# Kernel optimization log

Hardware: AMD Instinct MI355X
Metric: run time of the kernel (lower is better)

Reference implementation:

```python
import jax, jax.numpy as jnp
import numpy as np

jax.config.update("jax_enable_x64", True)

_FULL = 1 << 32
_MASK = _FULL - 1
_HALF = _FULL >> 1
_QUARTER = _HALF >> 1
_THREE_QUARTER = 3 * _QUARTER


def setup_inputs() -> dict:
    key = jax.random.key(0)
    num_symbols = 262144            # e.g. a 512x512 plane of {-1,+1} symbols
    num_bits = 2 * num_symbols      # compressed payload, ~2 bits/symbol budget
    payload_bits = jax.random.randint(key, (num_bits,), 0, 2, dtype=jnp.int64)
    return {
        "payload_bits": payload_bits,
        "total_freq": 4096,         # 1 << frequency_precision (12)
        "num_symbols": num_symbols,
        "context_bits": 8,
    }


def reference(payload_bits, total_freq, num_symbols, context_bits):
    bits = payload_bits.astype(jnp.int64)
    nb = bits.shape[0]
    num_states = 1 << context_bits
    smask = num_states - 1

    def read_bit(ptr):
        # _BitReader returns 0 past the end of the payload
        return jnp.where(ptr < nb, bits[jnp.clip(ptr, 0, nb - 1)], jnp.int64(0))

    # initial 32-bit code word
    idx32 = jnp.arange(32, dtype=jnp.int64)
    b32 = jnp.where(idx32 < nb, bits[jnp.clip(idx32, 0, nb - 1)], 0)
    code0 = jnp.sum(b32 << (31 - idx32))

    def renorm(carry):
        # E1/E2/E3 renormalization loop (bit-level, data dependent)
        def cond(c):
            low, high, code, ptr = c
            return (high < _HALF) | (low >= _HALF) | ((low >= _QUARTER) & (high < _THREE_QUARTER))

        def body(c):
            low, high, code, ptr = c
            sub = jnp.where(high < _HALF, jnp.int64(0),
                            jnp.where(low >= _HALF, jnp.int64(_HALF), jnp.int64(_QUARTER)))
            low = low - sub
            high = high - sub
            code = code - sub
            low = (low << 1) & _MASK
            high = ((high << 1) & _MASK) | 1
            code = ((code << 1) & _MASK) | read_bit(ptr)
            return (low, high, code, ptr + 1)

        return jax.lax.while_loop(cond, body, carry)

    def step(carry, _):
        low, high, code, ptr, state, count0, count1 = carry
        n0 = count0[state]
        n1 = count1[state]
        total = n0 + n1
        p0 = n0.astype(jnp.float64) / total.astype(jnp.float64)
        p0_freq = jnp.clip(jnp.rint(p0 * (total_freq - 2)) + 1.0, 1.0, float(total_freq - 1)).astype(jnp.int64)
        rng = high - low + 1                      # fits int64 (<= 2^32)
        scaled = ((code - low + 1) * total_freq - 1) // rng
        split = low + rng * p0_freq // total_freq
        bit = (scaled >= p0_freq).astype(jnp.int64)
        low2 = jnp.where(bit == 0, low, split)
        high2 = jnp.where(bit == 0, split - 1, high)
        low3, high3, code3, ptr3 = renorm((low2, high2, code, ptr))
        count0 = count0.at[state].add(1 - bit)
        count1 = count1.at[state].add(bit)
        state2 = ((state << 1) | bit) & smask
        return (low3, high3, code3, ptr3, state2, count0, count1), bit

    init = (
        jnp.int64(0),               # low
        jnp.int64(_MASK),           # high = 2^32 - 1
        code0.astype(jnp.int64),    # code
        jnp.int64(32),              # bit pointer (32 bits consumed)
        jnp.int64(0),               # context state
        jnp.ones(num_states, dtype=jnp.int64),  # count0 (Laplace init)
        jnp.ones(num_states, dtype=jnp.int64),  # count1
    )
    _, out_bits = jax.lax.scan(step, init, None, length=num_symbols)
    # map {0,1} -> {-1,+1} float32 symbols (reshape to bitstream.shape is metadata-only)
    return out_bits.astype(jnp.float32) * 2.0 - 1.0
```

## Files before the change

kernel.cpp:

```cpp
#include <hip/hip_runtime.h>


#define WORDS_LDS 16400
#define MAX_STATES 1024
#define OBITS_WORDS 8192

__device__ __forceinline__ long long ddiv_floor(long long n, long long d) {
    double qd = (double)n / (double)d;
    long long q = (long long)qd;
    long long r = n - q * d;
    q -= (r < 0);
    q += (r >= d);
    return q;
}

template<bool FAST>
__device__ __forceinline__ void decode_serial(
    const unsigned* __restrict__ words, unsigned* tab, unsigned* obits,
    const int* __restrict__ bits, int nb, int nwords,
    unsigned total_freq, int tf_shift, int num_symbols, int smask,
    unsigned pf0, float* __restrict__ out)
{
    const unsigned H = 0x80000000u;
    unsigned low = 0u, high = 0xFFFFFFFFu;
    unsigned code = words[0];
    unsigned long long bitbuf = (((unsigned long long)words[1]) << 32) | (unsigned long long)words[2];
    int navail = 64;
    unsigned pre = words[3];
    int widx = 4;

    const double tfm2d = (double)(total_freq - 2u);
    const int tfm1 = (int)(total_freq - 1u);
    const unsigned tfm2_2 = (total_freq - 2u) << 1;
    constexpr int EXT = FAST ? 14 : 30;

    int state = 0;
    unsigned n0 = 1u, n1 = 1u, pf = pf0;

    int wIdx = 0;
    unsigned wN0 = 1u, wN1 = 1u, wPf = pf0;

    unsigned obuf = 0u;

    for (int s = 0; s < num_symbols; ++s) {
        const int c0 = (state << 1) & smask;
        uint4 q = *reinterpret_cast<const uint4*>(tab + 2 * c0);

        if (navail <= 32) {
            bitbuf |= ((unsigned long long)pre) << (32 - navail);
            navail += 32;
            unsigned nxt = 0u;
            if (widx < WORDS_LDS) {
                nxt = words[widx];
            } else if (widx < nwords) {
                unsigned g = 0u;
                long long base = ((long long)widx) << 5;
                for (int j = 0; j < 32; ++j) {
                    long long idx = base + j;
                    int b = (idx < (long long)nb) ? (bits[idx] & 1) : 0;
                    g |= ((unsigned)b) << (31 - j);
                }
                nxt = g;
            }
            pre = nxt;
            ++widx;
        }

        const unsigned rngm1 = high - low;
        const unsigned long long P = (unsigned long long)pf * rngm1 + pf;
        const unsigned soff = FAST ? (unsigned)(P >> tf_shift)
                                   : (unsigned)ddiv_floor((long long)P, (long long)total_freq);
        const unsigned dlt = code - low;
        const int bit = (dlt >= soff) ? 1 : 0;
        const unsigned split = low + soff;
        low  = bit ? split : low;
        high = bit ? high : (split - 1u);
        obuf = (obuf << 1) | (unsigned)bit;

        const unsigned nn0 = n0 + (unsigned)(1 - bit);
        const unsigned nn1 = n1 + (unsigned)bit;
        unsigned pfn;
        if (FAST) {
            const unsigned t  = nn0 + nn1;
            const unsigned d2 = t << 1;
            const unsigned num2 = __umul24(tfm2_2, nn0) + t;
            const float qf = (float)num2 * __builtin_amdgcn_rcpf((float)d2);
            unsigned qi = (unsigned)qf;
            int r = (int)(num2 - __umul24(qi, d2));
            if (r < 0)          { qi -= 1u; r += (int)d2; }
            if (r >= (int)d2)   { qi += 1u; r -= (int)d2; }
            pfn = qi + 1u;
            if (__builtin_expect(r == 0, 0)) {
                asm volatile("");
                double p0d = (double)(int)nn0 / (double)(int)t;
                double pfd = rint(p0d * tfm2d) + 1.0;
                int pfi = (int)pfd;
                pfi = pfi < 1 ? 1 : (pfi > tfm1 ? tfm1 : pfi);
                pfn = (unsigned)pfi;
            }
        } else {
            double p0d = (double)(int)nn0 / (double)(int)(nn0 + nn1);
            double pfd = rint(p0d * tfm2d) + 1.0;
            int pfi = (int)pfd;
            pfi = pfi < 1 ? 1 : (pfi > tfm1 ? tfm1 : pfi);
            pfn = (unsigned)pfi;
        }

        const unsigned x = low ^ high;
        const int k = __builtin_clz(x);
        const unsigned aa = ~(low << (k + 1));
        const unsigned bb = (high << (k + 1)) | ((2u << k) - 1u);
        const int m = __builtin_clz(aa | bb);
        const int K = k + m;
        const unsigned sub = (m != 0) ? H : 0u;
        const unsigned ones = (1u << K) - 1u;
        const unsigned tE = (unsigned)(bitbuf >> (64 - EXT));
        const unsigned tK = tE >> (EXT - K);
        low  = (low << K) - sub;
        high = (high << K) + ones - sub;
        code = ((code << K) | tK) - sub;
        bitbuf <<= K;
        navail -= K;

        const int nidx = c0 | bit;
        const unsigned sw0 = bit ? q.z : q.x;
        const unsigned sw1 = bit ? q.w : q.y;
        const bool f2 = (nidx == wIdx);
        unsigned xn0 = f2 ? wN0 : sw0;
        unsigned xn1 = f2 ? wN1 : (sw1 & 0xFFFFFu);
        unsigned xpf = f2 ? wPf : (sw1 >> 20);

        *reinterpret_cast<uint2*>(tab + 2 * wIdx) = make_uint2(wN0, wN1 | (wPf << 20));
        wIdx = state; wN0 = nn0; wN1 = nn1; wPf = pfn;

        if (__builtin_expect(nidx == state, 0)) {
            asm volatile("");
            xn0 = nn0; xn1 = nn1; xpf = pfn;
        }
        state = nidx;
        n0 = xn0; n1 = xn1; pf = xpf;

        if ((s & 31) == 31) {
            int wo = s >> 5;
            if (wo < OBITS_WORDS) {
                obits[wo] = obuf;
            } else {
                int base = s & ~31;
                for (int j = 0; j < 32; ++j)
                    out[base + j] = ((obuf >> (31 - j)) & 1u) ? 1.0f : -1.0f;
            }
        }
    }
    if (num_symbols & 31) {
        int rem = num_symbols & 31;
        unsigned v = obuf << (32 - rem);
        int wo = num_symbols >> 5;
        if (wo < OBITS_WORDS) {
            obits[wo] = v;
        } else {
            int base = num_symbols & ~31;
            for (int j = 0; j < rem; ++j)
                out[base + j] = ((v >> (31 - j)) & 1u) ? 1.0f : -1.0f;
        }
    }
}

__global__ __launch_bounds__(256)
void EntropyDecoder_84928683311460_kernel(
    const int* __restrict__ bits,
    const int* __restrict__ tf_p,
    const int* __restrict__ ns_p,
    const int* __restrict__ cb_p,
    float* __restrict__ out,
    int nb)
{
    __shared__ unsigned words[WORDS_LDS];
    __shared__ __align__(16) unsigned tab[MAX_STATES * 2];
    __shared__ unsigned obits[OBITS_WORDS];

    const int tid = threadIdx.x;
    const unsigned total_freq = (unsigned)(*tf_p);
    const int num_symbols = *ns_p;
    const int context_bits = *cb_p;
    const int num_states = 1 << context_bits;
    const int smask = num_states - 1;
    const int nwords = (nb + 31) >> 5;

    for (int w = tid; w < WORDS_LDS; w += blockDim.x) {
        unsigned v = 0;
        int base = w << 5;
        if (base + 32 <= nb) {
            #pragma unroll
            for (int j = 0; j < 32; j += 4) {
                int4 b4 = *reinterpret_cast<const int4*>(bits + base + j);
                v |= ((unsigned)(b4.x & 1) << (31 - j))
                   | ((unsigned)(b4.y & 1) << (30 - j))
                   | ((unsigned)(b4.z & 1) << (29 - j))
                   | ((unsigned)(b4.w & 1) << (28 - j));
            }
        } else if (base < nb) {
            for (int j = 0; j < 32; ++j) {
                int idx = base + j;
                int b = (idx < nb) ? (bits[idx] & 1) : 0;
                v |= ((unsigned)b) << (31 - j);
            }
        }
        words[w] = v;
    }
    unsigned pf0;
    {
        double pfd = rint(0.5 * (double)(total_freq - 2u)) + 1.0;
        int t = (int)pfd;
        int tfm1 = (int)(total_freq - 1u);
        t = t < 1 ? 1 : (t > tfm1 ? tfm1 : t);
        pf0 = (unsigned)t;
    }
    for (int st = tid; st < num_states; st += blockDim.x) {
        tab[2 * st]     = 1u;
        tab[2 * st + 1] = 1u | (pf0 << 20);
    }
    __syncthreads();

    if (tid == 0) {
        const int tf_shift = 31 - __builtin_clz(total_freq);
        const bool pow2 = (total_freq & (total_freq - 1u)) == 0u;
        const unsigned long long bound =
            2ull * (unsigned long long)(total_freq - 2u) * (unsigned long long)(num_symbols + 1)
            + (unsigned long long)(num_symbols + 2);
        const bool fast = pow2 && total_freq >= 8u && total_freq <= 4096u
                          && bound < (1ull << 31);
        if (fast)
            decode_serial<true >(words, tab, obits, bits, nb, nwords, total_freq,
                                 tf_shift, num_symbols, smask, pf0, out);
        else
            decode_serial<false>(words, tab, obits, bits, nb, nwords, total_freq,
                                 tf_shift, num_symbols, smask, pf0, out);
    }
    __syncthreads();

    const int nwout = (num_symbols + 31) >> 5;
    const int npk = nwout < OBITS_WORDS ? nwout : OBITS_WORDS;
    for (int w = tid; w < npk; w += blockDim.x) {
        unsigned v = obits[w];
        int base = w << 5;
        if (base + 32 <= num_symbols) {
            #pragma unroll
            for (int j = 0; j < 32; j += 4) {
                float4 o;
                o.x = ((v >> (31 - j)) & 1u) ? 1.0f : -1.0f;
                o.y = ((v >> (30 - j)) & 1u) ? 1.0f : -1.0f;
                o.z = ((v >> (29 - j)) & 1u) ? 1.0f : -1.0f;
                o.w = ((v >> (28 - j)) & 1u) ? 1.0f : -1.0f;
                *reinterpret_cast<float4*>(out + base + j) = o;
            }
        } else {
            for (int j = 0; j < 32 && base + j < num_symbols; ++j)
                out[base + j] = ((v >> (31 - j)) & 1u) ? 1.0f : -1.0f;
        }
    }
}

extern "C" void kernel_launch(void* const* d_in, const int* in_sizes, int n_in,
                              void* d_out, int out_size, void* d_ws, size_t ws_size,
                              hipStream_t stream) {
    const int* bits = (const int*)d_in[0];
    const int* tf   = (const int*)d_in[1];
    const int* ns   = (const int*)d_in[2];
    const int* cb   = (const int*)d_in[3];
    float* out = (float*)d_out;
    int nb = in_sizes[0];

    hipLaunchKernelGGL(EntropyDecoder_84928683311460_kernel,
                       dim3(1), dim3(256), 0, stream,
                       bits, tf, ns, cb, out, nb);
}
```

Baseline: 79.84 ms.

## Keep context count table in wavefront registers via readlane instead of LDS

The fast path now runs on a full 64-lane wavefront. The 256-entry context count table is spread across lane registers (4 per lane) and read with readlane instead of LDS loads, with the pending write applied by a lane-select predicate on the next iteration. The decoder also tracks code-minus-low directly, which drops one subtraction from the serial chain. This targets LDS load latency on the serial per-symbol dependency chain. In exchange it adds 8 readlanes and selects per symbol, and it only applies when there are at most 256 states.

```diff
diff --git a/kernel.cpp b/kernel.cpp
--- a/kernel.cpp
+++ b/kernel.cpp
@@ -14,11 +14,160 @@
     return q;
 }
 
-template<bool FAST>
-__device__ __forceinline__ void decode_serial(
+__device__ __forceinline__ void decode_fast(
+    const unsigned* __restrict__ words, unsigned* obits,
+    const int* __restrict__ bits, int nb, int nwords,
+    unsigned total_freq, int tf_shift, int num_symbols, int smask,
+    unsigned pf0, float* __restrict__ out)
+{
+    const unsigned myLane = threadIdx.x & 63u;
+
+    unsigned a0 = 1u, a1 = 1u, a2 = 1u, a3 = 1u;
+    const unsigned bini = 1u | (pf0 << 20);
+    unsigned b0 = bini, b1 = bini, b2 = bini, b3 = bini;
+
+    unsigned low = 0u, high = 0xFFFFFFFFu;
+    unsigned dlt = words[0];
+    unsigned long long bitbuf = (((unsigned long long)words[1]) << 32)
+                              | (unsigned long long)words[2];
+    int unavail = 64;
+    unsigned pre = words[3];
+    int uwidx = 4;
+
+    const unsigned tfm2_2 = (total_freq - 2u) << 1;
+    const double tfm2d = (double)(total_freq - 2u);
+    const int tfm1 = (int)(total_freq - 1u);
+
+    int ustate = 0;
+    unsigned obuf = 0u;
+
+    bool pm0 = false, pm1 = false, pm2 = false, pm3 = false;
+    unsigned pN0 = 0u, pPK = 0u;
+
+    for (int s = 0; s < num_symbols; ++s) {
+        a0 = pm0 ? pN0 : a0;  a1 = pm1 ? pN0 : a1;
+        a2 = pm2 ? pN0 : a2;  a3 = pm3 ? pN0 : a3;
+        b0 = pm0 ? pPK : b0;  b1 = pm1 ? pPK : b1;
+        b2 = pm2 ? pPK : b2;  b3 = pm3 ? pPK : b3;
+
+        const int lane = ustate & 63;
+        const int ridx = ustate >> 6;
+        const unsigned ra0 = (unsigned)__builtin_amdgcn_readlane((int)a0, lane);
+        const unsigned ra1 = (unsigned)__builtin_amdgcn_readlane((int)a1, lane);
+        const unsigned ra2 = (unsigned)__builtin_amdgcn_readlane((int)a2, lane);
+        const unsigned ra3 = (unsigned)__builtin_amdgcn_readlane((int)a3, lane);
+        const unsigned rb0 = (unsigned)__builtin_amdgcn_readlane((int)b0, lane);
+        const unsigned rb1 = (unsigned)__builtin_amdgcn_readlane((int)b1, lane);
+        const unsigned rb2 = (unsigned)__builtin_amdgcn_readlane((int)b2, lane);
+        const unsigned rb3 = (unsigned)__builtin_amdgcn_readlane((int)b3, lane);
+        const unsigned rn0 = (ridx & 2) ? ((ridx & 1) ? ra3 : ra2)
+                                        : ((ridx & 1) ? ra1 : ra0);
+        const unsigned rpk = (ridx & 2) ? ((ridx & 1) ? rb3 : rb2)
+                                        : ((ridx & 1) ? rb1 : rb0);
+        const unsigned upf = rpk >> 20;
+        const unsigned un1 = rpk & 0xFFFFFu;
+
+        const unsigned rngm1 = high - low;
+        const unsigned long long P = (unsigned long long)upf * rngm1 + upf;
+        const unsigned soff = (unsigned)(P >> tf_shift);
+        const bool bt = (dlt >= soff);
+        const unsigned bitv = bt ? 1u : 0u;
+        const unsigned split = low + soff;
+        low  = bt ? split : low;
+        high = bt ? high : (split - 1u);
+        dlt  = bt ? (dlt - soff) : dlt;
+        obuf = (obuf << 1) | bitv;
+
+        const unsigned nn0 = rn0 + 1u - bitv;
+        const unsigned nn1 = un1 + bitv;
+        const unsigned t  = nn0 + nn1;
+        const unsigned d2 = t << 1;
+        const unsigned num2 = __umul24(tfm2_2, nn0) + t;
+        const float qf = (float)num2 * __builtin_amdgcn_rcpf((float)d2);
+        unsigned qi = (unsigned)qf;
+        int r = (int)(num2 - __umul24(qi, d2));
+        if (r < 0)        { qi -= 1u; r += (int)d2; }
+        if (r >= (int)d2) { qi += 1u; r -= (int)d2; }
+        unsigned pfn = qi + 1u;
+        if (__builtin_expect(__builtin_amdgcn_readfirstlane(r) == 0, 0)) {
+            double p0d = (double)(int)nn0 / (double)(int)t;
+            double pfd = rint(p0d * tfm2d) + 1.0;
+            int pfi = (int)pfd;
+            pfi = pfi < 1 ? 1 : (pfi > tfm1 ? tfm1 : pfi);
+            pfn = (unsigned)pfi;
+        }
+
+        const unsigned x = low ^ high;
+        const int k = __builtin_clz(x);
+        const unsigned aa  = ~(low << (k + 1));
+        const unsigned bbv = (high << (k + 1)) | ((2u << k) - 1u);
+        const int m = __builtin_clz(aa | bbv);
+        const int K = k + m;
+        const unsigned sub = (m != 0) ? 0x80000000u : 0u;
+        const unsigned ones = (1u << K) - 1u;
+        const unsigned tE = (unsigned)(bitbuf >> 50);
+        const unsigned tK = tE >> (14 - K);
+        low  = (low << K) - sub;
+        high = (high << K) + ones - sub;
+        dlt  = (dlt << K) | tK;
+        bitbuf <<= K;
+
+        const bool sel = (myLane == (unsigned)lane);
+        pm0 = sel && (ridx == 0);  pm1 = sel && (ridx == 1);
+        pm2 = sel && (ridx == 2);  pm3 = sel && (ridx == 3);
+        pN0 = nn0;
+        pPK = nn1 | (pfn << 20);
+
+        const int ubit = __builtin_amdgcn_readfirstlane((int)bitv);
+        ustate = ((ustate << 1) | ubit) & smask;
+        unavail -= __builtin_amdgcn_readfirstlane(K);
+        if (unavail <= 32) {
+            bitbuf |= ((unsigned long long)pre) << (32 - unavail);
+            unavail += 32;
+            unsigned nxt = 0u;
+            if (uwidx < WORDS_LDS) {
+                nxt = words[uwidx];
+            } else if (uwidx < nwords) {
+                unsigned g = 0u;
+                long long base = ((long long)uwidx) << 5;
+                for (int j = 0; j < 32; ++j) {
+                    long long idx = base + j;
+                    int b = (idx < (long long)nb) ? (bits[idx] & 1) : 0;
+                    g |= ((unsigned)b) << (31 - j);
+                }
+                nxt = g;
+            }
+            pre = nxt;
+            ++uwidx;
+        }
+        if ((s & 31) == 31) {
+            int wo = s >> 5;
+            if (wo < OBITS_WORDS) {
+                obits[wo] = obuf;
+            } else {
+                int base = s & ~31;
+                for (int j = 0; j < 32; ++j)
+                    out[base + j] = ((obuf >> (31 - j)) & 1u) ? 1.0f : -1.0f;
+            }
+        }
+    }
+    if (num_symbols & 31) {
+        int rem = num_symbols & 31;
+        unsigned v = obuf << (32 - rem);
+        int wo = num_symbols >> 5;
+        if (wo < OBITS_WORDS) obits[wo] = v;
+        else {
+            int base = num_symbols & ~31;
+            for (int j = 0; j < rem; ++j)
+                out[base + j] = ((v >> (31 - j)) & 1u) ? 1.0f : -1.0f;
+        }
+    }
+}
+
+__device__ void decode_serial_slow(
     const unsigned* __restrict__ words, unsigned* tab, unsigned* obits,
     const int* __restrict__ bits, int nb, int nwords,
-    unsigned total_freq, int tf_shift, int num_symbols, int smask,
+    unsigned total_freq, int num_symbols, int smask,
     unsigned pf0, float* __restrict__ out)
 {
     const unsigned H = 0x80000000u;
@@ -31,28 +180,22 @@
 
     const double tfm2d = (double)(total_freq - 2u);
     const int tfm1 = (int)(total_freq - 1u);
-    const unsigned tfm2_2 = (total_freq - 2u) << 1;
-    constexpr int EXT = FAST ? 14 : 30;
 
     int state = 0;
     unsigned n0 = 1u, n1 = 1u, pf = pf0;
-
     int wIdx = 0;
     unsigned wN0 = 1u, wN1 = 1u, wPf = pf0;
-
     unsigned obuf = 0u;
 
     for (int s = 0; s < num_symbols; ++s) {
         const int c0 = (state << 1) & smask;
         uint4 q = *reinterpret_cast<const uint4*>(tab + 2 * c0);
-
         if (navail <= 32) {
             bitbuf |= ((unsigned long long)pre) << (32 - navail);
             navail += 32;
             unsigned nxt = 0u;
-            if (widx < WORDS_LDS) {
-                nxt = words[widx];
-            } else if (widx < nwords) {
+            if (widx < WORDS_LDS) nxt = words[widx];
+            else if (widx < nwords) {
                 unsigned g = 0u;
                 long long base = ((long long)widx) << 5;
                 for (int j = 0; j < 32; ++j) {
@@ -65,11 +208,9 @@
             pre = nxt;
             ++widx;
         }
-
         const unsigned rngm1 = high - low;
         const unsigned long long P = (unsigned long long)pf * rngm1 + pf;
-        const unsigned soff = FAST ? (unsigned)(P >> tf_shift)
-                                   : (unsigned)ddiv_floor((long long)P, (long long)total_freq);
+        const unsigned soff = (unsigned)ddiv_floor((long long)P, (long long)total_freq);
         const unsigned dlt = code - low;
         const int bit = (dlt >= soff) ? 1 : 0;
         const unsigned split = low + soff;
@@ -79,43 +220,22 @@
 
         const unsigned nn0 = n0 + (unsigned)(1 - bit);
         const unsigned nn1 = n1 + (unsigned)bit;
-        unsigned pfn;
-        if (FAST) {
-            const unsigned t  = nn0 + nn1;
-            const unsigned d2 = t << 1;
-            const unsigned num2 = __umul24(tfm2_2, nn0) + t;
-            const float qf = (float)num2 * __builtin_amdgcn_rcpf((float)d2);
-            unsigned qi = (unsigned)qf;
-            int r = (int)(num2 - __umul24(qi, d2));
-            if (r < 0)          { qi -= 1u; r += (int)d2; }
-            if (r >= (int)d2)   { qi += 1u; r -= (int)d2; }
-            pfn = qi + 1u;
-            if (__builtin_expect(r == 0, 0)) {
-                asm volatile("");
-                double p0d = (double)(int)nn0 / (double)(int)t;
-                double pfd = rint(p0d * tfm2d) + 1.0;
-                int pfi = (int)pfd;
-                pfi = pfi < 1 ? 1 : (pfi > tfm1 ? tfm1 : pfi);
-                pfn = (unsigned)pfi;
-            }
-        } else {
-            double p0d = (double)(int)nn0 / (double)(int)(nn0 + nn1);
-            double pfd = rint(p0d * tfm2d) + 1.0;
-            int pfi = (int)pfd;
-            pfi = pfi < 1 ? 1 : (pfi > tfm1 ? tfm1 : pfi);
-            pfn = (unsigned)pfi;
-        }
+        double p0d = (double)(int)nn0 / (double)(int)(nn0 + nn1);
+        double pfd = rint(p0d * tfm2d) + 1.0;
+        int pfi = (int)pfd;
+        pfi = pfi < 1 ? 1 : (pfi > tfm1 ? tfm1 : pfi);
+        unsigned pfn = (unsigned)pfi;
 
         const unsigned x = low ^ high;
         const int k = __builtin_clz(x);
         const unsigned aa = ~(low << (k + 1));
-        const unsigned bb = (high << (k + 1)) | ((2u << k) - 1u);
-        const int m = __builtin_clz(aa | bb);
+        const unsigned bbv = (high << (k + 1)) | ((2u << k) - 1u);
+        const int m = __builtin_clz(aa | bbv);
         const int K = k + m;
         const unsigned sub = (m != 0) ? H : 0u;
         const unsigned ones = (1u << K) - 1u;
-        const unsigned tE = (unsigned)(bitbuf >> (64 - EXT));
-        const unsigned tK = tE >> (EXT - K);
+        const unsigned tE = (unsigned)(bitbuf >> 34);
+        const unsigned tK = tE >> (30 - K);
         low  = (low << K) - sub;
         high = (high << K) + ones - sub;
         code = ((code << K) | tK) - sub;
@@ -129,10 +249,8 @@
         unsigned xn0 = f2 ? wN0 : sw0;
         unsigned xn1 = f2 ? wN1 : (sw1 & 0xFFFFFu);
         unsigned xpf = f2 ? wPf : (sw1 >> 20);
-
         *reinterpret_cast<uint2*>(tab + 2 * wIdx) = make_uint2(wN0, wN1 | (wPf << 20));
         wIdx = state; wN0 = nn0; wN1 = nn1; wPf = pfn;
-
         if (__builtin_expect(nidx == state, 0)) {
             asm volatile("");
             xn0 = nn0; xn1 = nn1; xpf = pfn;
@@ -142,9 +260,8 @@
 
         if ((s & 31) == 31) {
             int wo = s >> 5;
-            if (wo < OBITS_WORDS) {
-                obits[wo] = obuf;
-            } else {
+            if (wo < OBITS_WORDS) obits[wo] = obuf;
+            else {
                 int base = s & ~31;
                 for (int j = 0; j < 32; ++j)
                     out[base + j] = ((obuf >> (31 - j)) & 1u) ? 1.0f : -1.0f;
@@ -155,9 +272,8 @@
         int rem = num_symbols & 31;
         unsigned v = obuf << (32 - rem);
         int wo = num_symbols >> 5;
-        if (wo < OBITS_WORDS) {
-            obits[wo] = v;
-        } else {
+        if (wo < OBITS_WORDS) obits[wo] = v;
+        else {
             int base = num_symbols & ~31;
             for (int j = 0; j < rem; ++j)
                 out[base + j] = ((v >> (31 - j)) & 1u) ? 1.0f : -1.0f;
@@ -221,20 +337,24 @@
     }
     __syncthreads();
 
-    if (tid == 0) {
-        const int tf_shift = 31 - __builtin_clz(total_freq);
-        const bool pow2 = (total_freq & (total_freq - 1u)) == 0u;
-        const unsigned long long bound =
-            2ull * (unsigned long long)(total_freq - 2u) * (unsigned long long)(num_symbols + 1)
-            + (unsigned long long)(num_symbols + 2);
-        const bool fast = pow2 && total_freq >= 8u && total_freq <= 4096u
-                          && bound < (1ull << 31);
-        if (fast)
-            decode_serial<true >(words, tab, obits, bits, nb, nwords, total_freq,
-                                 tf_shift, num_symbols, smask, pf0, out);
-        else
-            decode_serial<false>(words, tab, obits, bits, nb, nwords, total_freq,
-                                 tf_shift, num_symbols, smask, pf0, out);
+    const int tf_shift = 31 - __builtin_clz(total_freq);
+    const bool pow2 = (total_freq & (total_freq - 1u)) == 0u;
+    const unsigned long long bound =
+        2ull * (unsigned long long)(total_freq - 2u) * (unsigned long long)(num_symbols + 1)
+        + (unsigned long long)(num_symbols + 2);
+    const bool fast = pow2 && total_freq >= 8u && total_freq <= 4096u
+                      && bound < (1ull << 31) && num_states <= 256;
+
+    if (fast) {
+        if (tid < 64) {
+            decode_fast(words, obits, bits, nb, nwords, total_freq, tf_shift,
+                        num_symbols, smask, pf0, out);
+        }
+    } else {
+        if (tid == 0) {
+            decode_serial_slow(words, tab, obits, bits, nb, nwords, total_freq,
+                               num_symbols, smask, pf0, out);
+        }
     }
     __syncthreads();
 
```

After: 87.04 ms. 1.09x slower.

## Add specialized fast serial decoder with two-step context prefetch and branchless refill

Applied to the files above, without the earlier changes.

Adds a dedicated fast decode path that prefetches both possible next-next context table entries one step ahead, so the table load leaves the serial dependency chain. The path also keeps code-minus-low directly instead of code, refills the bit buffer without branches, preloads the next word, and unrolls 32 symbols per output word. Forwarding from the previous two updates handles table read-after-write hazards. The path only runs under tighter guards on state count, symbol count and payload size, and falls back to the slow path otherwise. This adds register pressure and some correctness risk in the hazard handling.

```diff
diff --git a/kernel.cpp b/kernel.cpp
--- a/kernel.cpp
+++ b/kernel.cpp
@@ -14,11 +14,124 @@
     return q;
 }
 
-template<bool FAST>
-__device__ __forceinline__ void decode_serial(
+__device__ __forceinline__ void decode_fast(
+    const unsigned* __restrict__ words, unsigned* tab, unsigned* obits,
+    unsigned total_freq, int tf_shift, int num_symbols, int smask, unsigned pf0)
+{
+    const unsigned H = 0x80000000u;
+    unsigned low = 0u, high = 0xFFFFFFFFu;
+    unsigned dlt = words[0];
+    unsigned long long bitbuf = (((unsigned long long)words[1]) << 32)
+                              | (unsigned long long)words[2];
+    int unavail = 64;
+    unsigned pre = words[3];
+    int widx = 4;
+    unsigned wnext = words[4];
+
+    const unsigned tfm2_2 = (total_freq - 2u) << 1;
+    const double tfm2d = (double)(total_freq - 2u);
+    const int tfm1 = (int)(total_freq - 1u);
+
+    int st = 0, stP = -1;
+    unsigned entN0 = 1u, entPK = 1u | (pf0 << 20);
+    unsigned P0n0 = 1u, P0pk = entPK;
+    unsigned P1n0 = 1u, P1pk = entPK;
+    unsigned uN0p = 0u, uPKp = 0u;
+
+    const int iters = num_symbols >> 5;
+    for (int it = 0; it < iters; ++it) {
+        unsigned obuf = 0u;
+        #pragma unroll
+        for (int u = 0; u < 32; ++u) {
+            const int gbase = ((st << 2) & smask) * 2;
+            const uint4 Ga = *reinterpret_cast<const uint4*>(tab + gbase);
+            const uint4 Gb = *reinterpret_cast<const uint4*>(tab + gbase + 4);
+
+            const unsigned pf  = entPK >> 20;
+            const unsigned n1v = entPK & 0xFFFFFu;
+            const unsigned n0v = entN0;
+            const unsigned rngm1 = high - low;
+            const unsigned long long P = (unsigned long long)pf * rngm1 + pf;
+            const unsigned soff = (unsigned)(P >> tf_shift);
+            const bool bt = (dlt >= soff);
+            const unsigned bitv = bt ? 1u : 0u;
+            const unsigned split = low + soff;
+            low  = bt ? split : low;
+            high = bt ? high : (split - 1u);
+            dlt  = bt ? (dlt - soff) : dlt;
+            obuf = (obuf << 1) | bitv;
+
+            const unsigned nn0 = n0v + 1u - bitv;
+            const unsigned nn1 = n1v + bitv;
+            const unsigned tt  = nn0 + nn1;
+            const unsigned d2  = tt << 1;
+            const unsigned num2 = __umul24(tfm2_2, nn0) + tt;
+            const float qf = (float)num2 * __builtin_amdgcn_rcpf((float)d2);
+            unsigned qi = (unsigned)qf;
+            int r = (int)(num2 - __umul24(qi, d2));
+            if (r < 0)        { qi -= 1u; r += (int)d2; }
+            if (r >= (int)d2) { qi += 1u; r -= (int)d2; }
+            unsigned pfn = qi + 1u;
+            if (__builtin_expect(__builtin_amdgcn_readfirstlane(r) == 0, 0)) {
+                asm volatile("");
+                double p0d = (double)(int)nn0 / (double)(int)tt;
+                double pfd = rint(p0d * tfm2d) + 1.0;
+                int pfi = (int)pfd;
+                pfi = pfi < 1 ? 1 : (pfi > tfm1 ? tfm1 : pfi);
+                pfn = (unsigned)pfi;
+            }
+            const unsigned npk = nn1 | (pfn << 20);
+
+            const unsigned x = low ^ high;
+            const int k = __builtin_clz(x);
+            const unsigned aa   = ~(low << (k + 1));
+            const unsigned bbv2 = (high << (k + 1)) | ((2u << k) - 1u);
+            const int m = __builtin_clz(aa | bbv2);
+            const int K = k + m;
+            const unsigned sub  = (m != 0) ? H : 0u;
+            const unsigned ones = (1u << K) - 1u;
+            const unsigned tK = ((unsigned)(bitbuf >> 50)) >> (14 - K);
+            low  = (low << K) - sub;
+            high = (high << K) + ones - sub;
+            dlt  = (dlt << K) | tK;
+            bitbuf <<= K;
+            unavail -= K;
+
+            const bool need = (unavail <= 32);
+            const unsigned long long ins =
+                (((unsigned long long)pre) << 32) >> (unavail & 63);
+            bitbuf |= need ? ins : 0ull;
+            unavail += need ? 32 : 0;
+            pre = need ? wnext : pre;
+            widx += need ? 1 : 0;
+            const int widxc = widx < (WORDS_LDS - 1) ? widx : (WORDS_LDS - 1);
+            wnext = words[widxc];
+
+            *reinterpret_cast<uint2*>(tab + 2 * st) = make_uint2(nn0, npk);
+
+            const int stN = ((st << 1) | (int)bitv) & smask;
+            unsigned en0 = bt ? P1n0 : P0n0;
+            unsigned epk = bt ? P1pk : P0pk;
+            if (__builtin_expect(stN == st || stN == stP, 0)) {
+                asm volatile("");
+                en0 = (stN == st) ? nn0 : uN0p;
+                epk = (stN == st) ? npk : uPKp;
+            }
+            P0n0 = bt ? Gb.x : Ga.x;  P0pk = bt ? Gb.y : Ga.y;
+            P1n0 = bt ? Gb.z : Ga.z;  P1pk = bt ? Gb.w : Ga.w;
+
+            uN0p = nn0; uPKp = npk;
+            stP = st; st = stN;
+            entN0 = en0; entPK = epk;
+        }
+        obits[it] = obuf;
+    }
+}
+
+__device__ void decode_serial_slow(
     const unsigned* __restrict__ words, unsigned* tab, unsigned* obits,
     const int* __restrict__ bits, int nb, int nwords,
-    unsigned total_freq, int tf_shift, int num_symbols, int smask,
+    unsigned total_freq, int num_symbols, int smask,
     unsigned pf0, float* __restrict__ out)
 {
     const unsigned H = 0x80000000u;
@@ -31,28 +144,22 @@
 
     const double tfm2d = (double)(total_freq - 2u);
     const int tfm1 = (int)(total_freq - 1u);
-    const unsigned tfm2_2 = (total_freq - 2u) << 1;
-    constexpr int EXT = FAST ? 14 : 30;
 
     int state = 0;
     unsigned n0 = 1u, n1 = 1u, pf = pf0;
-
     int wIdx = 0;
     unsigned wN0 = 1u, wN1 = 1u, wPf = pf0;
-
     unsigned obuf = 0u;
 
     for (int s = 0; s < num_symbols; ++s) {
         const int c0 = (state << 1) & smask;
         uint4 q = *reinterpret_cast<const uint4*>(tab + 2 * c0);
-
         if (navail <= 32) {
             bitbuf |= ((unsigned long long)pre) << (32 - navail);
             navail += 32;
             unsigned nxt = 0u;
-            if (widx < WORDS_LDS) {
-                nxt = words[widx];
-            } else if (widx < nwords) {
+            if (widx < WORDS_LDS) nxt = words[widx];
+            else if (widx < nwords) {
                 unsigned g = 0u;
                 long long base = ((long long)widx) << 5;
                 for (int j = 0; j < 32; ++j) {
@@ -65,11 +172,9 @@
             pre = nxt;
             ++widx;
         }
-
         const unsigned rngm1 = high - low;
         const unsigned long long P = (unsigned long long)pf * rngm1 + pf;
-        const unsigned soff = FAST ? (unsigned)(P >> tf_shift)
-                                   : (unsigned)ddiv_floor((long long)P, (long long)total_freq);
+        const unsigned soff = (unsigned)ddiv_floor((long long)P, (long long)total_freq);
         const unsigned dlt = code - low;
         const int bit = (dlt >= soff) ? 1 : 0;
         const unsigned split = low + soff;
@@ -79,43 +184,22 @@
 
         const unsigned nn0 = n0 + (unsigned)(1 - bit);
         const unsigned nn1 = n1 + (unsigned)bit;
-        unsigned pfn;
-        if (FAST) {
-            const unsigned t  = nn0 + nn1;
-            const unsigned d2 = t << 1;
-            const unsigned num2 = __umul24(tfm2_2, nn0) + t;
-            const float qf = (float)num2 * __builtin_amdgcn_rcpf((float)d2);
-            unsigned qi = (unsigned)qf;
-            int r = (int)(num2 - __umul24(qi, d2));
-            if (r < 0)          { qi -= 1u; r += (int)d2; }
-            if (r >= (int)d2)   { qi += 1u; r -= (int)d2; }
-            pfn = qi + 1u;
-            if (__builtin_expect(r == 0, 0)) {
-                asm volatile("");
-                double p0d = (double)(int)nn0 / (double)(int)t;
-                double pfd = rint(p0d * tfm2d) + 1.0;
-                int pfi = (int)pfd;
-                pfi = pfi < 1 ? 1 : (pfi > tfm1 ? tfm1 : pfi);
-                pfn = (unsigned)pfi;
-            }
-        } else {
-            double p0d = (double)(int)nn0 / (double)(int)(nn0 + nn1);
-            double pfd = rint(p0d * tfm2d) + 1.0;
-            int pfi = (int)pfd;
-            pfi = pfi < 1 ? 1 : (pfi > tfm1 ? tfm1 : pfi);
-            pfn = (unsigned)pfi;
-        }
+        double p0d = (double)(int)nn0 / (double)(int)(nn0 + nn1);
+        double pfd = rint(p0d * tfm2d) + 1.0;
+        int pfi = (int)pfd;
+        pfi = pfi < 1 ? 1 : (pfi > tfm1 ? tfm1 : pfi);
+        unsigned pfn = (unsigned)pfi;
 
         const unsigned x = low ^ high;
         const int k = __builtin_clz(x);
         const unsigned aa = ~(low << (k + 1));
-        const unsigned bb = (high << (k + 1)) | ((2u << k) - 1u);
-        const int m = __builtin_clz(aa | bb);
+        const unsigned bbv = (high << (k + 1)) | ((2u << k) - 1u);
+        const int m = __builtin_clz(aa | bbv);
         const int K = k + m;
         const unsigned sub = (m != 0) ? H : 0u;
         const unsigned ones = (1u << K) - 1u;
-        const unsigned tE = (unsigned)(bitbuf >> (64 - EXT));
-        const unsigned tK = tE >> (EXT - K);
+        const unsigned tE = (unsigned)(bitbuf >> 34);
+        const unsigned tK = tE >> (30 - K);
         low  = (low << K) - sub;
         high = (high << K) + ones - sub;
         code = ((code << K) | tK) - sub;
@@ -129,10 +213,8 @@
         unsigned xn0 = f2 ? wN0 : sw0;
         unsigned xn1 = f2 ? wN1 : (sw1 & 0xFFFFFu);
         unsigned xpf = f2 ? wPf : (sw1 >> 20);
-
         *reinterpret_cast<uint2*>(tab + 2 * wIdx) = make_uint2(wN0, wN1 | (wPf << 20));
         wIdx = state; wN0 = nn0; wN1 = nn1; wPf = pfn;
-
         if (__builtin_expect(nidx == state, 0)) {
             asm volatile("");
             xn0 = nn0; xn1 = nn1; xpf = pfn;
@@ -142,9 +224,8 @@
 
         if ((s & 31) == 31) {
             int wo = s >> 5;
-            if (wo < OBITS_WORDS) {
-                obits[wo] = obuf;
-            } else {
+            if (wo < OBITS_WORDS) obits[wo] = obuf;
+            else {
                 int base = s & ~31;
                 for (int j = 0; j < 32; ++j)
                     out[base + j] = ((obuf >> (31 - j)) & 1u) ? 1.0f : -1.0f;
@@ -155,9 +236,8 @@
         int rem = num_symbols & 31;
         unsigned v = obuf << (32 - rem);
         int wo = num_symbols >> 5;
-        if (wo < OBITS_WORDS) {
-            obits[wo] = v;
-        } else {
+        if (wo < OBITS_WORDS) obits[wo] = v;
+        else {
             int base = num_symbols & ~31;
             for (int j = 0; j < rem; ++j)
                 out[base + j] = ((v >> (31 - j)) & 1u) ? 1.0f : -1.0f;
@@ -221,20 +301,28 @@
     }
     __syncthreads();
 
-    if (tid == 0) {
-        const int tf_shift = 31 - __builtin_clz(total_freq);
-        const bool pow2 = (total_freq & (total_freq - 1u)) == 0u;
-        const unsigned long long bound =
-            2ull * (unsigned long long)(total_freq - 2u) * (unsigned long long)(num_symbols + 1)
-            + (unsigned long long)(num_symbols + 2);
-        const bool fast = pow2 && total_freq >= 8u && total_freq <= 4096u
-                          && bound < (1ull << 31);
-        if (fast)
-            decode_serial<true >(words, tab, obits, bits, nb, nwords, total_freq,
-                                 tf_shift, num_symbols, smask, pf0, out);
-        else
-            decode_serial<false>(words, tab, obits, bits, nb, nwords, total_freq,
-                                 tf_shift, num_symbols, smask, pf0, out);
+    const int tf_shift = 31 - __builtin_clz(total_freq);
+    const bool pow2 = (total_freq & (total_freq - 1u)) == 0u;
+    const unsigned long long bound =
+        2ull * (unsigned long long)(total_freq - 2u) * (unsigned long long)(num_symbols + 1)
+        + (unsigned long long)(num_symbols + 2);
+    const bool fast = pow2 && total_freq >= 8u && total_freq <= 4096u
+                      && bound < (1ull << 31)
+                      && num_states >= 4 && num_states <= 256
+                      && (num_symbols & 31) == 0
+                      && num_symbols <= OBITS_WORDS * 32
+                      && nwords <= 16384;
+
+    if (fast) {
+        if (tid == 0) {
+            decode_fast(words, tab, obits, total_freq, tf_shift,
+                        num_symbols, smask, pf0);
+        }
+    } else {
+        if (tid == 0) {
+            decode_serial_slow(words, tab, obits, bits, nb, nwords, total_freq,
+                               num_symbols, smask, pf0, out);
+        }
     }
     __syncthreads();
 
```

Result: slower. 84.91 ms (+6.3%).
